# Kernel tuning notes

Measured on AMD Instinct MI355X. Metric: run time of the kernel, lower is better.

The kernel has to match this reference:

```python
import jax, jax.numpy as jnp
import numpy as np

B, S, D, V = 2, 2048, 1024, 32000
EPS_LN = 1e-5
EPS_BN = 1e-5


def setup_inputs() -> dict:
    key = jax.random.key(0)
    ks = jax.random.split(key, 8)
    s = lambda k, shape: jax.random.normal(k, shape, jnp.float32) * 0.02
    return dict(
        X=jax.random.randint(ks[0], (B, S), 0, V, dtype=jnp.int32),
        emb=s(ks[1], (V, D)),
        w_hg=s(ks[2], (D, 2 * D)),            # minGRU to_hidden_and_gate (bias-free)
        conv_w=s(ks[3], (D, D, 3)),           # Conv1d OIW
        conv_b=jnp.zeros((D,), jnp.float32),
        bn_g=jnp.ones((D,), jnp.float32), bn_b=jnp.zeros((D,), jnp.float32),
        ln_g=jnp.ones((D,), jnp.float32), ln_b=jnp.zeros((D,), jnp.float32),
        w1=s(ks[4], (D, 2 * D)), b1=jnp.zeros((2 * D,), jnp.float32),
        w2=s(ks[5], (2 * D, 2 * D)), b2=jnp.zeros((2 * D,), jnp.float32),
        w3=s(ks[6], (2 * D, V)), b3=jnp.zeros((V,), jnp.float32),
    )


def _log_g(x):
    # log of g(x) = where(x>=0, x+0.5, sigmoid(x))
    return jnp.where(x >= 0, jnp.log(jax.nn.relu(x) + 0.5), -jax.nn.softplus(-x))


def _min_gru(x, w_hg):
    # Heinsen log-space associative scan (lucidrains minGRU, expansion=1)
    hg = x @ w_hg                              # [B,S,2D]
    hidden, gate = jnp.split(hg, 2, axis=-1)
    log_coeffs = -jax.nn.softplus(gate)        # log(1 - z)
    log_values = -jax.nn.softplus(-gate) + _log_g(hidden)  # log z + log h~
    a_star = jnp.cumsum(log_coeffs, axis=1)
    log_h = a_star + jax.lax.cumlogsumexp(log_values - a_star, axis=1)
    return jnp.exp(log_h)                      # [B,S,D]


def reference(X, emb, w_hg, conv_w, conv_b, bn_g, bn_b, ln_g, ln_b,
              w1, b1, w2, b2, w3, b3):
    x = emb[X]                                 # [B,S,D]
    shortcut = x
    h = _min_gru(x, w_hg)                      # dropout rate 0 -> identity
    mu = jnp.mean(h, axis=-1, keepdims=True)
    var = jnp.mean((h - mu) ** 2, axis=-1, keepdims=True)
    h = (h - mu) / jnp.sqrt(var + EPS_LN) * ln_g + ln_b
    x = h + shortcut
    xc = jnp.transpose(x, (0, 2, 1))           # [B,D,S]
    xc = jax.lax.conv_general_dilated(
        xc, conv_w, window_strides=(1,), padding=[(1, 1)],
        dimension_numbers=('NCW', 'OIW', 'NCW')) + conv_b[None, :, None]
    m = jnp.mean(xc, axis=(0, 2), keepdims=True)       # BN training-mode stats
    v = jnp.mean((xc - m) ** 2, axis=(0, 2), keepdims=True)
    xc = (xc - m) / jnp.sqrt(v + EPS_BN) * bn_g[None, :, None] + bn_b[None, :, None]
    x = jnp.transpose(xc, (0, 2, 1))           # [B,S,D]
    x = jax.nn.relu(x @ w1 + b1)
    x = jax.nn.relu(x @ w2 + b2)
    return x @ w3 + b3                         # [B,S,V]
```

## Files before the change

### kernel.cpp

```cpp
#include <hip/hip_runtime.h>
#include <hip/hip_bf16.h>

#define B_  2
#define S_  2048
#define D_  1024
#define V_  32000
#define BS_ 4096

typedef __attribute__((ext_vector_type(4))) float f32x4;
typedef __attribute__((ext_vector_type(8))) short short8;
typedef unsigned long long u64;
typedef unsigned short u16;

__device__ __forceinline__ u16 f2bf(float x) {
  unsigned int u = __float_as_uint(x);
  u += 0x7FFFu + ((u >> 16) & 1u);
  return (u16)(u >> 16);
}
__device__ __forceinline__ u64 pack4bf(float a, float b, float c, float d) {
  return (u64)f2bf(a) | ((u64)f2bf(b) << 16) | ((u64)f2bf(c) << 32) | ((u64)f2bf(d) << 48);
}

#define GLOAD_LDS16(g, l) __builtin_amdgcn_global_load_lds( \
    (const __attribute__((address_space(1))) void*)(g),     \
    (__attribute__((address_space(3))) void*)(l), 16, 0, 0)

__device__ __forceinline__ unsigned lds_addr32(const void* p) {
  return (unsigned)(uintptr_t)(const __attribute__((address_space(3))) void*)p;
}
__device__ __forceinline__ short8 ds_read128(unsigned a) {
  short8 r;
  asm volatile("ds_read_b128 %0, %1" : "=v"(r) : "v"(a));
  return r;
}

template<bool RELU, bool BF16OUT, bool HASBIAS>
__global__ __launch_bounds__(256) void gemm_bt(
    const u16* __restrict__ A, const u16* __restrict__ Bt,
    const float* __restrict__ bias, void* __restrict__ Cout,
    int M, int N, int K)
{
  __shared__ __attribute__((aligned(16))) u16 Alds[128 * 64];
  __shared__ __attribute__((aligned(16))) u16 Blds[128 * 64];
  const int tid = threadIdx.x;
  const int w = tid >> 6, l = tid & 63;
  const int wr = w >> 1, wc = w & 1;
  const int m0 = blockIdx.y * 128, n0 = blockIdx.x * 128;
  const int lr = l >> 3, lc = l & 7;
  const int fr = l & 15, fq = l >> 4;

  const u16* Ag = A + (size_t)(m0 + w * 8 + lr) * K + lc * 8;
  const u16* Bg = Bt + (size_t)(n0 + w * 8 + lr) * K + lc * 8;

  f32x4 acc[4][4];
#pragma unroll
  for (int i = 0; i < 4; ++i)
#pragma unroll
    for (int j = 0; j < 4; ++j) acc[i][j] = {0.f, 0.f, 0.f, 0.f};

  for (int kt = 0; kt < K; kt += 64) {
#pragma unroll
    for (int r = 0; r < 4; ++r) {
      GLOAD_LDS16(Ag + (size_t)(r * 32) * K + kt, &Alds[(r * 32 + w * 8) * 64]);
      GLOAD_LDS16(Bg + (size_t)(r * 32) * K + kt, &Blds[(r * 32 + w * 8) * 64]);
    }
    __syncthreads();
#pragma unroll
    for (int ks = 0; ks < 2; ++ks) {
      short8 af[4], bfv[4];
#pragma unroll
      for (int i = 0; i < 4; ++i)
        af[i] = *reinterpret_cast<const short8*>(
            &Alds[(wr * 64 + i * 16 + fr) * 64 + ks * 32 + fq * 8]);
#pragma unroll
      for (int j = 0; j < 4; ++j)
        bfv[j] = *reinterpret_cast<const short8*>(
            &Blds[(wc * 64 + j * 16 + fr) * 64 + ks * 32 + fq * 8]);
#pragma unroll
      for (int i = 0; i < 4; ++i)
#pragma unroll
        for (int j = 0; j < 4; ++j)
          acc[i][j] = __builtin_amdgcn_mfma_f32_16x16x32_bf16(af[i], bfv[j], acc[i][j], 0, 0, 0);
    }
    __syncthreads();
  }

  const int row0 = m0 + wr * 64 + fq * 4;
  const int col0 = n0 + wc * 64 + fr;
#pragma unroll
  for (int j = 0; j < 4; ++j) {
    const int col = col0 + j * 16;
    const float bv = HASBIAS ? bias[col] : 0.f;
#pragma unroll
    for (int i = 0; i < 4; ++i) {
#pragma unroll
      for (int r = 0; r < 4; ++r) {
        const int row = row0 + i * 16 + r;
        float v = acc[i][j][r] + bv;
        if (RELU) v = fmaxf(v, 0.f);
        if (BF16OUT) ((u16*)Cout)[(size_t)row * N + col] = f2bf(v);
        else         ((float*)Cout)[(size_t)row * N + col] = v;
      }
    }
  }
}

#define BARRIER() __builtin_amdgcn_s_barrier()
#define WAITL0_PIN() do { asm volatile("s_waitcnt lgkmcnt(0)" ::: "memory"); \
                          __builtin_amdgcn_sched_barrier(0); } while (0)
#define SCHED_WALL() __builtin_amdgcn_sched_barrier(0)
#define VMCNTN(n) asm volatile("s_waitcnt vmcnt(" #n ")" ::: "memory")

template<bool RELU, bool BF16OUT, bool HASBIAS>
__global__ __launch_bounds__(512, 2) void gemm256_bt(
    const u16* __restrict__ A, const u16* __restrict__ Bt,
    const float* __restrict__ bias, void* __restrict__ Cout,
    int M, int N, int K, int CW)
{
  __shared__ __attribute__((aligned(16))) u16 LDS[65536];
  const int tid = threadIdx.x;
  const int w = tid >> 6, l = tid & 63;
  const int wr = w >> 2, wc = w & 3;
  const int fr = l & 15, fq = l >> 4;
  const unsigned ldsb = lds_addr32(&LDS[0]);

  const int MTt = M >> 8;
  const int bpc = MTt * CW;
  const int chunk = blockIdx.x / bpc, rem = blockIdx.x % bpc;
  const int m0 = (rem % MTt) << 8;
  const int n0 = ((chunk * CW) + rem / MTt) << 8;

  const int NT = K >> 6;
  const u16* Abase = A + (size_t)m0 * K;
  const u16* Bbase = Bt + (size_t)n0 * K;

  const int rq_[2] = { w * 16 + (l >> 3), w * 16 + 8 + (l >> 3) };
  const int gq_[2] = { (l & 7) ^ (rq_[0] & 7), (l & 7) ^ (rq_[1] & 7) };
  const u16* gA[2][2];
  const u16* gB[2][2];
#pragma unroll
  for (int h = 0; h < 2; ++h)
#pragma unroll
    for (int q = 0; q < 2; ++q) {
      gA[h][q] = Abase + (size_t)(h * 128 + rq_[q]) * K + gq_[q] * 8;
      gB[h][q] = Bbase + (size_t)(h * 128 + rq_[q]) * K + gq_[q] * 8;
    }

  const int swz0 = ((0 * 4 + fq) ^ (fr & 7)) * 16;
  const int swz1 = ((1 * 4 + fq) ^ (fr & 7)) * 16;
  const unsigned aB = ldsb + 16384u * wr + 128u * fr;
  const unsigned bB = ldsb + 32768u + 16384u * (wc >> 1) + 128u * ((wc & 1) * 64 + fr);
  const unsigned bA00 = aB + swz0,           bA01 = aB + swz1;
  const unsigned bA10 = aB + 65536u + swz0,  bA11 = aB + 65536u + swz1;
  const unsigned bB00 = bB + swz0,           bB01 = bB + swz1;
  const unsigned bB10 = bB + 65536u + swz0,  bB11 = bB + 65536u + swz1;

#define STAGE_A(h, t, buf) do { _Pragma("unroll")                            \
  for (int q_ = 0; q_ < 2; ++q_)                                             \
    GLOAD_LDS16(gA[h][q_] + (size_t)(t) * 64,                                \
                &LDS[(((buf) * 4) + (h)) * 8192 + (w * 128 + q_ * 64) * 8]); \
} while (0)
#define STAGE_B(h, t, buf) do { _Pragma("unroll")                            \
  for (int q_ = 0; q_ < 2; ++q_)                                             \
    GLOAD_LDS16(gB[h][q_] + (size_t)(t) * 64,                                \
                &LDS[(((buf) * 4) + 2 + (h)) * 8192 + (w * 128 + q_ * 64) * 8]); \
} while (0)

#define RDA_(arr, k0, k1, Q) do { _Pragma("unroll")                          \
  for (int i_ = 0; i_ < 4; ++i_) {                                           \
    arr[i_][0] = ds_read128((k0) + (Q) * 8192 + i_ * 2048);                  \
    arr[i_][1] = ds_read128((k1) + (Q) * 8192 + i_ * 2048);                  \
  } } while (0)
#define RDB_(arr, k0, k1, JQ) do { _Pragma("unroll")                         \
  for (int j_ = 0; j_ < 2; ++j_) {                                           \
    arr[j_][0] = ds_read128((k0) + (JQ) * 4096 + j_ * 2048);                 \
    arr[j_][1] = ds_read128((k1) + (JQ) * 4096 + j_ * 2048);                 \
  } } while (0)

#define MFMA_Q(arrA, arrB, itb, jtb) do { _Pragma("unroll")                  \
  for (int i_ = 0; i_ < 4; ++i_)                                             \
    _Pragma("unroll")                                                        \
    for (int j_ = 0; j_ < 2; ++j_)                                           \
      _Pragma("unroll")                                                      \
      for (int ks_ = 0; ks_ < 2; ++ks_)                                      \
        acc[(itb) + i_][(jtb) + j_] = __builtin_amdgcn_mfma_f32_16x16x32_bf16( \
            arrA[i_][ks_], arrB[j_][ks_], acc[(itb) + i_][(jtb) + j_], 0, 0, 0); \
} while (0)

  f32x4 acc[8][4];
#pragma unroll
  for (int i = 0; i < 8; ++i)
#pragma unroll
    for (int j = 0; j < 4; ++j) acc[i][j] = {0.f, 0.f, 0.f, 0.f};

  short8 a0[4][2], a1[4][2], b0[2][2], b1[2][2];

  STAGE_A(0, 0, 0); STAGE_A(1, 0, 0); STAGE_B(0, 0, 0); STAGE_B(1, 0, 0);
  STAGE_B(0, 1, 1); STAGE_A(0, 1, 1);
  VMCNTN(4);
  BARRIER();
  RDA_(a0, bA00, bA01, 0);
  RDB_(b0, bB00, bB01, 0);
  BARRIER();

#define TILE(t, cb, nb) do {                                                 \
                                                                     \
  WAITL0_PIN();                                                              \
  RDB_(b1, bB##cb##0, bB##cb##1, 1);                                         \
  if ((t) + 1 < NT) STAGE_A(1, (t) + 1, nb);                                 \
  SCHED_WALL();                                                              \
  __builtin_amdgcn_s_setprio(1); MFMA_Q(a0, b0, 0, 0); __builtin_amdgcn_s_setprio(0); \
  BARRIER();                                                                 \
                                                                     \
  WAITL0_PIN();                                                              \
  RDA_(a1, bA##cb##0, bA##cb##1, 1);                                         \
  if ((t) + 1 < NT) STAGE_B(1, (t) + 1, nb);                                 \
  SCHED_WALL();                                                              \
  __builtin_amdgcn_s_setprio(1); MFMA_Q(a0, b1, 0, 2); __builtin_amdgcn_s_setprio(0); \
  BARRIER();                                                                 \
                                                                     \
  WAITL0_PIN();                                                              \
  if ((t) + 2 < NT) STAGE_B(0, (t) + 2, cb);                                 \
  SCHED_WALL();                                                              \
  __builtin_amdgcn_s_setprio(1); MFMA_Q(a1, b1, 4, 2); __builtin_amdgcn_s_setprio(0); \
  BARRIER();                                                                 \
                                                                     \
  if ((t) + 2 < NT) STAGE_A(0, (t) + 2, cb);                                 \
  SCHED_WALL();                                                              \
  __builtin_amdgcn_s_setprio(1); MFMA_Q(a1, b0, 4, 0); __builtin_amdgcn_s_setprio(0); \
  if ((t) + 2 < NT) { VMCNTN(4); } else { VMCNTN(0); }                       \
  BARRIER();                \
  if ((t) + 1 < NT) {                                                        \
    RDA_(a0, bA##nb##0, bA##nb##1, 0);                                       \
    RDB_(b0, bB##nb##0, bB##nb##1, 0);                                       \
  }                                                                          \
  BARRIER();                                                                 \
} while (0)

  for (int t = 0; t < NT; t += 2) {
    TILE(t, 0, 1);
    TILE(t + 1, 1, 0);
  }
#undef TILE

  float* lf = (float*)(void*)(&LDS[0]) + (size_t)w * 1152;
  const int row_base = m0 + wr * 128;
  const int col_base = n0 + wc * 64;
  float bvv[4];
#pragma unroll
  for (int jt = 0; jt < 4; ++jt)
    bvv[jt] = HASBIAS ? bias[col_base + jt * 16 + fr] : 0.f;
  const int er = l >> 4, ec = (l & 15) * 4;
#pragma unroll
  for (int it = 0; it < 8; ++it) {
#pragma unroll
    for (int jt = 0; jt < 4; ++jt)
#pragma unroll
      for (int rr = 0; rr < 4; ++rr)
        lf[(fq * 4 + rr) * 72 + jt * 16 + fr] = acc[it][jt][rr] + bvv[jt];
#pragma unroll
    for (int ch = 0; ch < 4; ++ch) {
      f32x4 vv = *(const f32x4*)&lf[(ch * 4 + er) * 72 + ec];
      if (RELU) {
        vv[0] = fmaxf(vv[0], 0.f); vv[1] = fmaxf(vv[1], 0.f);
        vv[2] = fmaxf(vv[2], 0.f); vv[3] = fmaxf(vv[3], 0.f);
      }
      const int grow = row_base + it * 16 + ch * 4 + er;
      if (BF16OUT) {
        *(u64*)(&((u16*)Cout)[(size_t)grow * N + col_base + ec]) =
            pack4bf(vv[0], vv[1], vv[2], vv[3]);
      } else {
        __builtin_nontemporal_store(vv,
            (f32x4*)(&((float*)Cout)[(size_t)grow * N + col_base + ec]));
      }
    }
  }
#undef STAGE_A
#undef STAGE_B
#undef RDA_
#undef RDB_
#undef MFMA_Q
}

__global__ __launch_bounds__(256) void transpose_f2b(
    const float* __restrict__ in, u16* __restrict__ out, int K, int N)
{
  __shared__ float t[32][33];
  const int n0 = blockIdx.x * 32, k0 = blockIdx.y * 32;
  const int r = threadIdx.x >> 5, cc = threadIdx.x & 31;
#pragma unroll
  for (int rr = 0; rr < 4; ++rr) {
    const int ki = rr * 8 + r;
    t[ki][cc] = in[(size_t)(k0 + ki) * N + n0 + cc];
  }
  __syncthreads();
#pragma unroll
  for (int rr = 0; rr < 4; ++rr) {
    const int ni = rr * 8 + r;
    out[(size_t)(n0 + ni) * K + k0 + cc] = f2bf(t[cc][ni]);
  }
}

__global__ __launch_bounds__(256) void convw_reorder(
    const float* __restrict__ cw, u16* __restrict__ out)
{
  const int gid = blockIdx.x * 256 + threadIdx.x;
  const int o = gid >> 10, i = gid & 1023;
  const float w0 = cw[(size_t)gid * 3 + 0];
  const float w1 = cw[(size_t)gid * 3 + 1];
  const float w2 = cw[(size_t)gid * 3 + 2];
  out[(size_t)o * 3072 + i]          = f2bf(w0);
  out[(size_t)o * 3072 + 1024 + i]   = f2bf(w1);
  out[(size_t)o * 3072 + 2048 + i]   = f2bf(w2);
}

__global__ __launch_bounds__(256) void gather_emb(
    const int* __restrict__ X, const float* __restrict__ emb, u16* __restrict__ xb)
{
  const int row = blockIdx.x;
  const int tok = X[row];
  const int d4 = threadIdx.x * 4;
  const float4 v = *reinterpret_cast<const float4*>(emb + (size_t)tok * D_ + d4);
  *(u64*)(&xb[(size_t)row * D_ + d4]) = pack4bf(v.x, v.y, v.z, v.w);
}

#define GRU_CP(hid_, gate_, h_, cp_) {                                   \
  const float t_ = __expf(-(gate_));                                     \
  const float z_ = 1.f / (1.f + t_);                                     \
  const float c_ = t_ * z_;                                              \
  const float g_ = ((hid_) >= 0.f) ? ((hid_) + 0.5f)                     \
                                   : (1.f / (1.f + __expf(-(hid_))));    \
  (h_) = c_ * (h_) + z_ * g_; (cp_) *= c_; }

#define GRU_NC(hid_, gate_, h_) {                                        \
  const float t_ = __expf(-(gate_));                                     \
  const float z_ = 1.f / (1.f + t_);                                     \
  const float g_ = ((hid_) >= 0.f) ? ((hid_) + 0.5f)                     \
                                   : (1.f / (1.f + __expf(-(hid_))));    \
  (h_) = (t_ * z_) * (h_) + z_ * g_; }

__global__ __launch_bounds__(256) void scan_partial(
    const float* __restrict__ hg, float* __restrict__ Cb, float* __restrict__ Vb)
{
  const int b = blockIdx.x >> 6, c = blockIdx.x & 63;
  const int d4 = threadIdx.x * 4;
  const float* base = hg + ((size_t)b * S_ + (size_t)c * 32) * (2 * D_);
  float h[4] = {0.f, 0.f, 0.f, 0.f}, cp[4] = {1.f, 1.f, 1.f, 1.f};
  for (int t = 0; t < 32; ++t) {
    const float4 hd = *reinterpret_cast<const float4*>(base + (size_t)t * (2 * D_) + d4);
    const float4 gt = *reinterpret_cast<const float4*>(base + (size_t)t * (2 * D_) + D_ + d4);
    GRU_CP(hd.x, gt.x, h[0], cp[0]); GRU_CP(hd.y, gt.y, h[1], cp[1]);
    GRU_CP(hd.z, gt.z, h[2], cp[2]); GRU_CP(hd.w, gt.w, h[3], cp[3]);
  }
  const size_t o = ((size_t)(b * 64 + c)) * D_ + d4;
  *(float4*)(Cb + o) = make_float4(cp[0], cp[1], cp[2], cp[3]);
  *(float4*)(Vb + o) = make_float4(h[0], h[1], h[2], h[3]);
}

__global__ void scan_carry(const float* __restrict__ Cb, const float* __restrict__ Vb,
                           float* __restrict__ Hs)
{
  const int gid = blockIdx.x * 256 + threadIdx.x;
  const int b = gid >> 10, d = gid & 1023;
  float h = 0.f;
  for (int c = 0; c < 64; ++c) {
    const size_t o = ((size_t)(b * 64 + c)) * D_ + d;
    Hs[o] = h;
    h = Cb[o] * h + Vb[o];
  }
}

__global__ __launch_bounds__(256) void scan_emit(
    const float* __restrict__ hg, const float* __restrict__ Hs,
    const int* __restrict__ X, const float* __restrict__ emb,
    const float* __restrict__ ln_g, const float* __restrict__ ln_b,
    u16* __restrict__ Aconv)
{
  __shared__ float red[4];
  const int b = blockIdx.x >> 6, c = blockIdx.x & 63;
  const int tid = threadIdx.x;
  const int w = tid >> 6, l = tid & 63;
  const int d4 = tid * 4;
  const float* base = hg + ((size_t)b * S_ + (size_t)c * 32) * (2 * D_);
  float h0, h1, h2, h3;
  {
    const float4 hs = *reinterpret_cast<const float4*>(Hs + ((size_t)(b * 64 + c)) * D_ + d4);
    h0 = hs.x; h1 = hs.y; h2 = hs.z; h3 = hs.w;
  }
  const float4 lg = *reinterpret_cast<const float4*>(ln_g + d4);
  const float4 lb = *reinterpret_cast<const float4*>(ln_b + d4);

  for (int t = 0; t < 32; ++t) {
    const int s = c * 32 + t;
    const float4 hd = *reinterpret_cast<const float4*>(base + (size_t)t * (2 * D_) + d4);
    const float4 gt = *reinterpret_cast<const float4*>(base + (size_t)t * (2 * D_) + D_ + d4);
    GRU_NC(hd.x, gt.x, h0); GRU_NC(hd.y, gt.y, h1);
    GRU_NC(hd.z, gt.z, h2); GRU_NC(hd.w, gt.w, h3);

    float sm = h0 + h1 + h2 + h3;
#pragma unroll
    for (int m = 1; m < 64; m <<= 1) sm += __shfl_xor(sm, m);
    __syncthreads();
    if (l == 0) red[w] = sm;
    __syncthreads();
    const float mu = (red[0] + red[1] + red[2] + red[3]) * (1.f / (float)D_);
    float q = (h0 - mu) * (h0 - mu) + (h1 - mu) * (h1 - mu) +
              (h2 - mu) * (h2 - mu) + (h3 - mu) * (h3 - mu);
#pragma unroll
    for (int m = 1; m < 64; m <<= 1) q += __shfl_xor(q, m);
    __syncthreads();
    if (l == 0) red[w] = q;
    __syncthreads();
    const float var = (red[0] + red[1] + red[2] + red[3]) * (1.f / (float)D_);
    const float rstd = rsqrtf(var + 1e-5f);

    const int tok = X[b * S_ + s];
    const float4 e = *reinterpret_cast<const float4*>(emb + (size_t)tok * D_ + d4);
    const float x0 = (h0 - mu) * rstd * lg.x + lb.x + e.x;
    const float x1 = (h1 - mu) * rstd * lg.y + lb.y + e.y;
    const float x2 = (h2 - mu) * rstd * lg.z + lb.z + e.z;
    const float x3 = (h3 - mu) * rstd * lg.w + lb.w + e.w;
    const u64 pk = pack4bf(x0, x1, x2, x3);

    const size_t row = (size_t)b * S_ + s;
    *(u64*)(&Aconv[row * 3072 + D_ + d4]) = pk;
    if (s + 1 < S_) *(u64*)(&Aconv[(row + 1) * 3072 + d4]) = pk;
    if (s > 0)      *(u64*)(&Aconv[(row - 1) * 3072 + 2 * D_ + d4]) = pk;
    if (s == 0)       *(u64*)(&Aconv[row * 3072 + d4]) = 0ull;
    if (s == S_ - 1)  *(u64*)(&Aconv[row * 3072 + 2 * D_ + d4]) = 0ull;
  }
}

__global__ __launch_bounds__(256) void bn_partial(
    const float* __restrict__ cv, float* __restrict__ ps, float* __restrict__ pq)
{
  const int blk = blockIdx.x;
  const int c4 = threadIdx.x * 4;
  float s0 = 0, s1 = 0, s2 = 0, s3 = 0, q0 = 0, q1 = 0, q2 = 0, q3 = 0;
  for (int r = 0; r < 64; ++r) {
    const float4 v = *reinterpret_cast<const float4*>(cv + ((size_t)blk * 64 + r) * D_ + c4);
    s0 += v.x; s1 += v.y; s2 += v.z; s3 += v.w;
    q0 += v.x * v.x; q1 += v.y * v.y; q2 += v.z * v.z; q3 += v.w * v.w;
  }
  *(float4*)(ps + (size_t)blk * D_ + c4) = make_float4(s0, s1, s2, s3);
  *(float4*)(pq + (size_t)blk * D_ + c4) = make_float4(q0, q1, q2, q3);
}

__global__ void bn_finalize(const float* __restrict__ ps, const float* __restrict__ pq,
                            const float* __restrict__ bn_g, const float* __restrict__ bn_b,
                            float* __restrict__ scale, float* __restrict__ shift)
{
  const int c = blockIdx.x * 256 + threadIdx.x;
  float s = 0.f, q = 0.f;
  for (int blk = 0; blk < 64; ++blk) { s += ps[(size_t)blk * D_ + c]; q += pq[(size_t)blk * D_ + c]; }
  const float m = s * (1.f / (float)BS_);
  const float var = q * (1.f / (float)BS_) - m * m;
  const float rs = rsqrtf(var + 1e-5f);
  const float sc = bn_g[c] * rs;
  scale[c] = sc;
  shift[c] = bn_b[c] - m * sc;
}

__global__ __launch_bounds__(256) void bn_apply(
    const float* __restrict__ cv, const float* __restrict__ scale,
    const float* __restrict__ shift, u16* __restrict__ out)
{
  const size_t idx = ((size_t)blockIdx.x * 256 + threadIdx.x) * 4;
  const int c = (int)(idx & 1023);
  const float4 v = *reinterpret_cast<const float4*>(cv + idx);
  const float4 sc = *reinterpret_cast<const float4*>(scale + c);
  const float4 sh = *reinterpret_cast<const float4*>(shift + c);
  *(u64*)(&out[idx]) = pack4bf(v.x * sc.x + sh.x, v.y * sc.y + sh.y,
                               v.z * sc.z + sh.z, v.w * sc.w + sh.w);
}

extern "C" void kernel_launch(void* const* d_in, const int* in_sizes, int n_in,
                              void* d_out, int out_size, void* d_ws, size_t ws_size,
                              hipStream_t stream)
{
  const int*   X      = (const int*)d_in[0];
  const float* emb    = (const float*)d_in[1];
  const float* w_hg   = (const float*)d_in[2];
  const float* conv_w = (const float*)d_in[3];
  const float* bn_g   = (const float*)d_in[5];
  const float* bn_b   = (const float*)d_in[6];
  const float* ln_g   = (const float*)d_in[7];
  const float* ln_b   = (const float*)d_in[8];
  const float* w1     = (const float*)d_in[9];
  const float* b1     = (const float*)d_in[10];
  const float* w2     = (const float*)d_in[11];
  const float* b2     = (const float*)d_in[12];
  const float* w3     = (const float*)d_in[13];
  const float* b3     = (const float*)d_in[14];
  float* out = (float*)d_out;
  char* ws = (char*)d_ws;

  const size_t OFF_A4    = 0;
  const size_t BASE      = 16777216;
  const size_t OFF_W3T   = BASE;
  const size_t OFF_WHGT  = BASE;
  const size_t OFF_W1T   = BASE + 4194304;
  const size_t OFF_W2T   = OFF_W1T + 4194304;
  const size_t OFF_WCVT  = OFF_W2T + 8388608;
  const size_t OFF_XBF   = OFF_WCVT + 6291456;
  const size_t OFF_HG    = OFF_XBF + 8388608;
  const size_t OFF_CB    = OFF_HG + 33554432;
  const size_t OFF_VB    = OFF_CB + 524288;
  const size_t OFF_HS    = OFF_VB + 524288;
  const size_t OFF_ACONV = OFF_HS + 524288;
  const size_t OFF_CVO   = OFF_ACONV + 25165824;
  const size_t OFF_A2    = OFF_CVO + 16777216;
  const size_t OFF_A3    = OFF_A2 + 8388608;
  const size_t OFF_BNS   = OFF_A3 + 16777216;
  const size_t OFF_BNQ   = OFF_BNS + 262144;
  const size_t OFF_SC    = OFF_BNQ + 262144;
  const size_t OFF_SH    = OFF_SC + 4096;
  (void)in_sizes; (void)n_in; (void)out_size; (void)ws_size;

  u16*   WHGT = (u16*)(ws + OFF_WHGT);
  u16*   W1T  = (u16*)(ws + OFF_W1T);
  u16*   W2T  = (u16*)(ws + OFF_W2T);
  u16*   W3T  = (u16*)(ws + OFF_W3T);
  u16*   WCVT = (u16*)(ws + OFF_WCVT);
  u16*   XBF  = (u16*)(ws + OFF_XBF);
  float* HG   = (float*)(ws + OFF_HG);
  float* CB   = (float*)(ws + OFF_CB);
  float* VB   = (float*)(ws + OFF_VB);
  float* HS   = (float*)(ws + OFF_HS);
  u16*   ACONV= (u16*)(ws + OFF_ACONV);
  float* CVO  = (float*)(ws + OFF_CVO);
  u16*   A2   = (u16*)(ws + OFF_A2);
  u16*   A3   = (u16*)(ws + OFF_A3);
  u16*   A4   = (u16*)(ws + OFF_A4);
  float* BNS  = (float*)(ws + OFF_BNS);
  float* BNQ  = (float*)(ws + OFF_BNQ);
  float* SC   = (float*)(ws + OFF_SC);
  float* SH   = (float*)(ws + OFF_SH);

  transpose_f2b<<<dim3(2048 / 32, 1024 / 32), 256, 0, stream>>>(w_hg, WHGT, 1024, 2048);
  transpose_f2b<<<dim3(2048 / 32, 1024 / 32), 256, 0, stream>>>(w1,   W1T,  1024, 2048);
  transpose_f2b<<<dim3(2048 / 32, 2048 / 32), 256, 0, stream>>>(w2,   W2T,  2048, 2048);
  convw_reorder<<<4096, 256, 0, stream>>>(conv_w, WCVT);

  gather_emb<<<BS_, 256, 0, stream>>>(X, emb, XBF);

  gemm_bt<false, false, false><<<dim3(2048 / 128, BS_ / 128), 256, 0, stream>>>(
      XBF, WHGT, nullptr, HG, BS_, 2048, 1024);

  scan_partial<<<B_ * 64, 256, 0, stream>>>(HG, CB, VB);
  scan_carry<<<8, 256, 0, stream>>>(CB, VB, HS);
  scan_emit<<<B_ * 64, 256, 0, stream>>>(HG, HS, X, emb, ln_g, ln_b, ACONV);

  gemm_bt<false, false, false><<<dim3(1024 / 128, BS_ / 128), 256, 0, stream>>>(
      ACONV, WCVT, nullptr, CVO, BS_, 1024, 3072);

  bn_partial<<<64, 256, 0, stream>>>(CVO, BNS, BNQ);
  bn_finalize<<<4, 256, 0, stream>>>(BNS, BNQ, bn_g, bn_b, SC, SH);
  bn_apply<<<4096, 256, 0, stream>>>(CVO, SC, SH, A2);

  gemm_bt<true, true, true><<<dim3(2048 / 128, BS_ / 128), 256, 0, stream>>>(
      A2, W1T, b1, A3, BS_, 2048, 1024);
  gemm_bt<true, true, true><<<dim3(2048 / 128, BS_ / 128), 256, 0, stream>>>(
      A3, W2T, b2, A4, BS_, 2048, 2048);

  transpose_f2b<<<dim3(V_ / 32, 2048 / 32), 256, 0, stream>>>(w3, W3T, 2048, V_);
  gemm256_bt<false, false, true><<<dim3((BS_ / 256) * (V_ / 256)), 512, 0, stream>>>(
      A4, W3T, b3, out, BS_, V_, 2048, 16);
}
```

Baseline: 1.015 ms.

## Restructure vocab GEMM schedule, XCD-strided block mapping, and epilogue padding

```diff
diff --git a/kernel.cpp b/kernel.cpp
--- a/kernel.cpp
+++ b/kernel.cpp
@@ -30,7 +30,7 @@
 }
 __device__ __forceinline__ short8 ds_read128(unsigned a) {
   short8 r;
-  asm volatile("ds_read_b128 %0, %1" : "=v"(r) : "v"(a));
+  asm volatile("ds_read_b128 %0, %1" : "=&v"(r) : "v"(a));
   return r;
 }
 
@@ -108,14 +108,13 @@
 #define BARRIER() __builtin_amdgcn_s_barrier()
 #define WAITL0_PIN() do { asm volatile("s_waitcnt lgkmcnt(0)" ::: "memory"); \
                           __builtin_amdgcn_sched_barrier(0); } while (0)
-#define SCHED_WALL() __builtin_amdgcn_sched_barrier(0)
 #define VMCNTN(n) asm volatile("s_waitcnt vmcnt(" #n ")" ::: "memory")
 
 template<bool RELU, bool BF16OUT, bool HASBIAS>
 __global__ __launch_bounds__(512, 2) void gemm256_bt(
     const u16* __restrict__ A, const u16* __restrict__ Bt,
     const float* __restrict__ bias, void* __restrict__ Cout,
-    int M, int N, int K, int CW)
+    int M, int N, int K)
 {
   __shared__ __attribute__((aligned(16))) u16 LDS[65536];
   const int tid = threadIdx.x;
@@ -125,10 +124,11 @@
   const unsigned ldsb = lds_addr32(&LDS[0]);
 
   const int MTt = M >> 8;
-  const int bpc = MTt * CW;
-  const int chunk = blockIdx.x / bpc, rem = blockIdx.x % bpc;
-  const int m0 = (rem % MTt) << 8;
-  const int n0 = ((chunk * CW) + rem / MTt) << 8;
+  const int total = MTt * (N >> 8);
+  const int perx = total >> 3;
+  const int p = (blockIdx.x & 7) * perx + (blockIdx.x >> 3);
+  const int m0 = (p % MTt) << 8;
+  const int n0 = (p / MTt) << 8;
 
   const int NT = K >> 6;
   const u16* Abase = A + (size_t)m0 * K;
@@ -199,41 +199,32 @@
   STAGE_B(0, 1, 1); STAGE_A(0, 1, 1);
   VMCNTN(4);
   BARRIER();
-  RDA_(a0, bA00, bA01, 0);
-  RDB_(b0, bB00, bB01, 0);
-  BARRIER();
 
 #define TILE(t, cb, nb) do {                                                 \
-                                                                     \
-  WAITL0_PIN();                                                              \
-  RDB_(b1, bB##cb##0, bB##cb##1, 1);                                         \
+                                         \
+  RDA_(a0, bA##cb##0, bA##cb##1, 0);                                         \
+  RDB_(b0, bB##cb##0, bB##cb##1, 0);                                         \
   if ((t) + 1 < NT) STAGE_A(1, (t) + 1, nb);                                 \
-  SCHED_WALL();                                                              \
+  BARRIER(); WAITL0_PIN();                                                   \
   __builtin_amdgcn_s_setprio(1); MFMA_Q(a0, b0, 0, 0); __builtin_amdgcn_s_setprio(0); \
   BARRIER();                                                                 \
-                                                                     \
-  WAITL0_PIN();                                                              \
-  RDA_(a1, bA##cb##0, bA##cb##1, 1);                                         \
+                                            \
+  RDB_(b1, bB##cb##0, bB##cb##1, 1);                                         \
   if ((t) + 1 < NT) STAGE_B(1, (t) + 1, nb);                                 \
-  SCHED_WALL();                                                              \
+  BARRIER(); WAITL0_PIN();                                                   \
   __builtin_amdgcn_s_setprio(1); MFMA_Q(a0, b1, 0, 2); __builtin_amdgcn_s_setprio(0); \
   BARRIER();                                                                 \
-                                                                     \
-  WAITL0_PIN();                                                              \
+                                            \
+  RDA_(a1, bA##cb##0, bA##cb##1, 1);                                         \
   if ((t) + 2 < NT) STAGE_B(0, (t) + 2, cb);                                 \
-  SCHED_WALL();                                                              \
+  BARRIER(); WAITL0_PIN();                                                   \
   __builtin_amdgcn_s_setprio(1); MFMA_Q(a1, b1, 4, 2); __builtin_amdgcn_s_setprio(0); \
   BARRIER();                                                                 \
-                                                                     \
+                     \
   if ((t) + 2 < NT) STAGE_A(0, (t) + 2, cb);                                 \
-  SCHED_WALL();                                                              \
+  BARRIER(); WAITL0_PIN();                                                   \
   __builtin_amdgcn_s_setprio(1); MFMA_Q(a1, b0, 4, 0); __builtin_amdgcn_s_setprio(0); \
   if ((t) + 2 < NT) { VMCNTN(4); } else { VMCNTN(0); }                       \
-  BARRIER();                \
-  if ((t) + 1 < NT) {                                                        \
-    RDA_(a0, bA##nb##0, bA##nb##1, 0);                                       \
-    RDB_(b0, bB##nb##0, bB##nb##1, 0);                                       \
-  }                                                                          \
   BARRIER();                                                                 \
 } while (0)
 
@@ -243,7 +234,7 @@
   }
 #undef TILE
 
-  float* lf = (float*)(void*)(&LDS[0]) + (size_t)w * 1152;
+  float* lf = (float*)(void*)(&LDS[0]) + (size_t)w * 1056;
   const int row_base = m0 + wr * 128;
   const int col_base = n0 + wc * 64;
   float bvv[4];
@@ -257,10 +248,10 @@
     for (int jt = 0; jt < 4; ++jt)
 #pragma unroll
       for (int rr = 0; rr < 4; ++rr)
-        lf[(fq * 4 + rr) * 72 + jt * 16 + fr] = acc[it][jt][rr] + bvv[jt];
+        lf[(fq * 4 + rr) * 66 + jt * 16 + fr] = acc[it][jt][rr] + bvv[jt];
 #pragma unroll
     for (int ch = 0; ch < 4; ++ch) {
-      f32x4 vv = *(const f32x4*)&lf[(ch * 4 + er) * 72 + ec];
+      f32x4 vv = *(const f32x4*)&lf[(ch * 4 + er) * 66 + ec];
       if (RELU) {
         vv[0] = fmaxf(vv[0], 0.f); vv[1] = fmaxf(vv[1], 0.f);
         vv[2] = fmaxf(vv[2], 0.f); vv[3] = fmaxf(vv[3], 0.f);
@@ -270,8 +261,7 @@
         *(u64*)(&((u16*)Cout)[(size_t)grow * N + col_base + ec]) =
             pack4bf(vv[0], vv[1], vv[2], vv[3]);
       } else {
-        __builtin_nontemporal_store(vv,
-            (f32x4*)(&((float*)Cout)[(size_t)grow * N + col_base + ec]));
+        *(f32x4*)(&((float*)Cout)[(size_t)grow * N + col_base + ec]) = vv;
       }
     }
   }
@@ -565,5 +555,5 @@
 
   transpose_f2b<<<dim3(V_ / 32, 2048 / 32), 256, 0, stream>>>(w3, W3T, 2048, V_);
   gemm256_bt<false, false, true><<<dim3((BS_ / 256) * (V_ / 256)), 512, 0, stream>>>(
-      A4, W3T, b3, out, BS_, V_, 2048, 16);
-}
+      A4, W3T, b3, out, BS_, V_, 2048);
+}
```

Result: faster. 915.1 us (-9.8%).
